# Kernel optimization log

Measured on AMD Instinct MI355X. Metric: run time of the kernel, lower is better.

Reference implementation:

```python
import jax, jax.numpy as jnp
import numpy as np

HIDDEN = 1024

def setup_inputs() -> dict:
    key = jax.random.key(0)
    k1, k2, k3 = jax.random.split(key, 3)
    X = jax.random.normal(k1, (4, 2048, HIDDEN), dtype=jnp.float32)
    W = jax.random.normal(k2, (HIDDEN, 3 * HIDDEN), dtype=jnp.float32) * (1.0 / np.sqrt(HIDDEN))
    b = jax.random.normal(k3, (3 * HIDDEN,), dtype=jnp.float32) * 0.02
    return {"X": X, "W": W, "b": b}

def reference(X, W, b):
    D = X.shape[-1]
    # fused QKV projection: [B,S,3D]
    QKV = jnp.einsum('bsd,de->bse', X, W) + b
    Q, K, V = jnp.split(QKV, 3, axis=-1)
    # full attention scores [B,S,S]
    scores = jnp.einsum('bqd,bkd->bqk', Q, K) / jnp.sqrt(jnp.float32(D))
    attn = jax.nn.softmax(scores, axis=-1)
    out = jnp.einsum('bqk,bkd->bqd', attn, V)
    return out
```

## Files before the change

kernel.cpp:

```cpp
#include <hip/hip_runtime.h>

typedef unsigned short u16;
typedef unsigned int   u32;
typedef __attribute__((ext_vector_type(8)))  short bf16x8;
typedef __attribute__((ext_vector_type(16))) float f32x16;
typedef __attribute__((ext_vector_type(4)))  unsigned short us4;

__device__ __forceinline__ u16 f2bf(float f) {
    union { float f; u32 u; } v; v.f = f;
    u32 u = v.u;
    return (u16)((u + 0x7fffu + ((u >> 16) & 1u)) >> 16);
}
__device__ __forceinline__ float bf2f_lo(u32 p) {
    union { u32 u; float f; } t; t.u = p << 16; return t.f;
}
__device__ __forceinline__ float bf2f_hi(u32 p) {
    union { u32 u; float f; } t; t.u = p & 0xffff0000u; return t.f;
}

__device__ __forceinline__ void gload_lds16(const void* g, void* l) {
    __builtin_amdgcn_global_load_lds((const __attribute__((address_space(1))) u32*)g,
                                     (__attribute__((address_space(3))) u32*)l,
                                     16, 0, 0);
}


template<bool OUT_BF16, bool ADD_BIAS, bool VT_OUT, int MODE>
__global__ __launch_bounds__(256, 2)
void gemm256(const u16* __restrict__ A, int lda, size_t strA,
             const u16* __restrict__ B, int ldb, size_t strB,
             void* __restrict__ Cv, int ldc, size_t strC,
             const float* __restrict__ bias, int K, float alpha)
{
    __shared__ __align__(16) u16 As[256 * 32];
    __shared__ __align__(16) u16 Bs[128 * 32];

    const int tid  = threadIdx.x;
    const int w    = tid >> 6;
    const int lane = tid & 63;
    const int wm   = w >> 1, wn = w & 1;
    const int l31  = lane & 31, lh = lane >> 5;

    const u32 id = blockIdx.x;
    const u32 x  = id & 7, j = id >> 3;
    int mb, nb, bb;
    if (MODE == 0) { bb = 0;      mb = 8 * (j & 3) + x;       nb = j >> 2; }
    else           { bb = x >> 1; mb = 2 * (j & 3) + (x & 1); nb = j >> 2; }
    const int m0 = mb * 256, n0 = nb * 128;

    A += (size_t)bb * strA;
    B += (size_t)bb * strB;

    size_t goffA[4], goffB[2];
#pragma unroll
    for (int h = 0; h < 4; ++h) {
        const int c = h * 256 + w * 64 + lane;
        const int r = c >> 2;
        const int q = ((c & 3) - (r >> 1)) & 3;
        goffA[h] = (size_t)(m0 + r) * lda + q * 8;
    }
#pragma unroll
    for (int h = 0; h < 2; ++h) {
        const int c = h * 256 + w * 64 + lane;
        const int r = c >> 2;
        const int q = ((c & 3) - (r >> 1)) & 3;
        goffB[h] = (size_t)(n0 + r) * ldb + q * 8;
    }

    int offA[4][2], offB[2][2];
#pragma unroll
    for (int i = 0; i < 4; ++i) {
        const int ra = wm * 128 + i * 32 + l31;
#pragma unroll
        for (int ks = 0; ks < 2; ++ks)
            offA[i][ks] = (ra * 4 + ((ks * 2 + lh + (ra >> 1)) & 3)) * 16;
    }
#pragma unroll
    for (int jj = 0; jj < 2; ++jj) {
        const int rb = wn * 64 + jj * 32 + l31;
#pragma unroll
        for (int ks = 0; ks < 2; ++ks)
            offB[jj][ks] = (rb * 4 + ((ks * 2 + lh + (rb >> 1)) & 3)) * 16;
    }

    f32x16 acc[4][2] = {};

    for (int k0 = 0; k0 < K; k0 += 32) {
#pragma unroll
        for (int h = 0; h < 4; ++h)
            gload_lds16(A + goffA[h] + k0, (char*)As + (h * 256 + w * 64) * 16);
#pragma unroll
        for (int h = 0; h < 2; ++h)
            gload_lds16(B + goffB[h] + k0, (char*)Bs + (h * 256 + w * 64) * 16);
        __syncthreads();

        bf16x8 af[4][2], bfr[2][2];
#pragma unroll
        for (int i = 0; i < 4; ++i)
#pragma unroll
            for (int ks = 0; ks < 2; ++ks)
                af[i][ks] = *(const bf16x8*)((const char*)As + offA[i][ks]);
#pragma unroll
        for (int jj = 0; jj < 2; ++jj)
#pragma unroll
            for (int ks = 0; ks < 2; ++ks)
                bfr[jj][ks] = *(const bf16x8*)((const char*)Bs + offB[jj][ks]);

#pragma unroll
        for (int ks = 0; ks < 2; ++ks)
#pragma unroll
            for (int i = 0; i < 4; ++i)
#pragma unroll
                for (int jj = 0; jj < 2; ++jj)
                    acc[i][jj] = __builtin_amdgcn_mfma_f32_32x32x16_bf16(
                        af[i][ks], bfr[jj][ks], acc[i][jj], 0, 0, 0);
        __syncthreads();
    }

    float bval[2];
    if (ADD_BIAS) {
#pragma unroll
        for (int jj = 0; jj < 2; ++jj) bval[jj] = bias[n0 + wn * 64 + jj * 32 + l31];
    }
#pragma unroll
    for (int i = 0; i < 4; ++i) {
        const int rowb = m0 + wm * 128 + i * 32 + 4 * lh;
#pragma unroll
        for (int jj = 0; jj < 2; ++jj) {
            const int col = n0 + wn * 64 + jj * 32 + l31;
            if (VT_OUT) {
                const int b = rowb >> 11;
                u16* dst = (u16*)Cv + ((size_t)(b * 1024) + col) * 2048 + (rowb & 2047);
#pragma unroll
                for (int g = 0; g < 4; ++g) {
                    us4 o = { f2bf(acc[i][jj][4 * g + 0] + bval[jj]),
                              f2bf(acc[i][jj][4 * g + 1] + bval[jj]),
                              f2bf(acc[i][jj][4 * g + 2] + bval[jj]),
                              f2bf(acc[i][jj][4 * g + 3] + bval[jj]) };
                    *(us4*)(dst + 8 * g) = o;
                }
            } else {
#pragma unroll
                for (int r = 0; r < 16; ++r) {
                    const int row = rowb + (r & 3) + 8 * (r >> 2);
                    float v = acc[i][jj][r] * alpha;
                    if (ADD_BIAS) v += bval[jj];
                    if (OUT_BF16)
                        ((u16*)Cv)[(size_t)bb * strC + (size_t)row * ldc + col] = f2bf(v);
                    else
                        ((float*)Cv)[(size_t)bb * strC + (size_t)row * ldc + col] = v;
                }
            }
        }
    }
}

template<bool OUT_BF16>
__global__ __launch_bounds__(256)
void gemm128(const u16* __restrict__ A, int lda, size_t strA,
             const u16* __restrict__ B, int ldb, size_t strB,
             void* __restrict__ Cv, int ldc, size_t strC,
             int K, float alpha)
{
    __shared__ __align__(16) u16 As[128 * 32];
    __shared__ __align__(16) u16 Bs[128 * 32];

    const int tid  = threadIdx.x;
    const int w    = tid >> 6;
    const int lane = tid & 63;
    const int wm   = w >> 1, wn = w & 1;
    const int l31  = lane & 31, lh = lane >> 5;

    const u32 id = blockIdx.x;
    const u32 x  = id & 7, j = id >> 3;
    const int bb = x >> 1;
    const int mb = 2 * (int)(j & 7) + (int)(x & 1);
    const int nb = j >> 3;
    const int m0 = mb * 128, n0 = nb * 128;

    A += (size_t)bb * strA;
    B += (size_t)bb * strB;

    size_t goffA[2], goffB[2];
#pragma unroll
    for (int h = 0; h < 2; ++h) {
        const int c = h * 256 + w * 64 + lane;
        const int r = c >> 2;
        const int q = ((c & 3) - (r >> 1)) & 3;
        goffA[h] = (size_t)(m0 + r) * lda + q * 8;
        goffB[h] = (size_t)(n0 + r) * ldb + q * 8;
    }

    int offA[2][2], offB[2][2];
#pragma unroll
    for (int i = 0; i < 2; ++i) {
        const int ra = wm * 64 + i * 32 + l31;
        const int rb = wn * 64 + i * 32 + l31;
#pragma unroll
        for (int ks = 0; ks < 2; ++ks) {
            const int qq = ks * 2 + lh;
            offA[i][ks] = (ra * 4 + ((qq + (ra >> 1)) & 3)) * 16;
            offB[i][ks] = (rb * 4 + ((qq + (rb >> 1)) & 3)) * 16;
        }
    }

    f32x16 acc[2][2] = {};

    for (int k0 = 0; k0 < K; k0 += 32) {
        gload_lds16(A + goffA[0] + k0, (char*)As + (w * 64) * 16);
        gload_lds16(A + goffA[1] + k0, (char*)As + (256 + w * 64) * 16);
        gload_lds16(B + goffB[0] + k0, (char*)Bs + (w * 64) * 16);
        gload_lds16(B + goffB[1] + k0, (char*)Bs + (256 + w * 64) * 16);
        __syncthreads();

        bf16x8 af[2][2], bfr[2][2];
#pragma unroll
        for (int i = 0; i < 2; ++i)
#pragma unroll
            for (int ks = 0; ks < 2; ++ks) {
                af[i][ks]  = *(const bf16x8*)((const char*)As + offA[i][ks]);
                bfr[i][ks] = *(const bf16x8*)((const char*)Bs + offB[i][ks]);
            }
#pragma unroll
        for (int ks = 0; ks < 2; ++ks)
#pragma unroll
            for (int i = 0; i < 2; ++i)
#pragma unroll
                for (int jj = 0; jj < 2; ++jj)
                    acc[i][jj] = __builtin_amdgcn_mfma_f32_32x32x16_bf16(
                        af[i][ks], bfr[jj][ks], acc[i][jj], 0, 0, 0);
        __syncthreads();
    }

#pragma unroll
    for (int i = 0; i < 2; ++i) {
        const int rowb = m0 + wm * 64 + i * 32 + 4 * lh;
#pragma unroll
        for (int jj = 0; jj < 2; ++jj) {
            const int col = n0 + wn * 64 + jj * 32 + l31;
#pragma unroll
            for (int r = 0; r < 16; ++r) {
                const int row = rowb + (r & 3) + 8 * (r >> 2);
                float v = acc[i][jj][r] * alpha;
                if (OUT_BF16)
                    ((u16*)Cv)[(size_t)bb * strC + (size_t)row * ldc + col] = f2bf(v);
                else
                    ((float*)Cv)[(size_t)bb * strC + (size_t)row * ldc + col] = v;
            }
        }
    }
}

__global__ __launch_bounds__(256)
void convert_x(const float* __restrict__ X, u16* __restrict__ Xb, int n4)
{
    int i = blockIdx.x * blockDim.x + threadIdx.x;
    if (i < n4) {
        float4 v = ((const float4*)X)[i];
        us4 o = { f2bf(v.x), f2bf(v.y), f2bf(v.z), f2bf(v.w) };
        ((us4*)Xb)[i] = o;
    }
}

__global__ __launch_bounds__(256)
void transpose_w(const float* __restrict__ W, u16* __restrict__ Wt)
{
    __shared__ u16 t[64][65];
    const int k0 = blockIdx.x * 64, n0 = blockIdx.y * 64;
    const int tx = threadIdx.x, ty = threadIdx.y;
#pragma unroll
    for (int i = 0; i < 64; i += 4)
        t[ty + i][tx] = f2bf(W[(size_t)(k0 + ty + i) * 3072 + n0 + tx]);
    __syncthreads();
#pragma unroll
    for (int i = 0; i < 64; i += 4)
        Wt[(size_t)(n0 + ty + i) * 1024 + k0 + tx] = t[tx][ty + i];
}

__global__ __launch_bounds__(256)
void softmax_rows(u16* __restrict__ S)
{
    __shared__ float redm[4], reds[4];
    u16* sr = S + (size_t)blockIdx.x * 2048;
    const int t = threadIdx.x;

    uint4 raw = ((const uint4*)sr)[t];
    float xx[8];
    xx[0] = bf2f_lo(raw.x); xx[1] = bf2f_hi(raw.x);
    xx[2] = bf2f_lo(raw.y); xx[3] = bf2f_hi(raw.y);
    xx[4] = bf2f_lo(raw.z); xx[5] = bf2f_hi(raw.z);
    xx[6] = bf2f_lo(raw.w); xx[7] = bf2f_hi(raw.w);

    float mx = fmaxf(fmaxf(fmaxf(xx[0], xx[1]), fmaxf(xx[2], xx[3])),
                     fmaxf(fmaxf(xx[4], xx[5]), fmaxf(xx[6], xx[7])));
#pragma unroll
    for (int o = 32; o; o >>= 1) mx = fmaxf(mx, __shfl_xor(mx, o));
    if ((t & 63) == 0) redm[t >> 6] = mx;
    __syncthreads();
    mx = fmaxf(fmaxf(redm[0], redm[1]), fmaxf(redm[2], redm[3]));

    float e[8], s = 0.f;
#pragma unroll
    for (int k = 0; k < 8; ++k) { e[k] = __expf(xx[k] - mx); s += e[k]; }
#pragma unroll
    for (int o = 32; o; o >>= 1) s += __shfl_xor(s, o);
    if ((t & 63) == 0) reds[t >> 6] = s;
    __syncthreads();
    s = reds[0] + reds[1] + reds[2] + reds[3];
    const float inv = 1.0f / s;

    uint4 o4;
    o4.x = (u32)f2bf(e[0] * inv) | ((u32)f2bf(e[1] * inv) << 16);
    o4.y = (u32)f2bf(e[2] * inv) | ((u32)f2bf(e[3] * inv) << 16);
    o4.z = (u32)f2bf(e[4] * inv) | ((u32)f2bf(e[5] * inv) << 16);
    o4.w = (u32)f2bf(e[6] * inv) | ((u32)f2bf(e[7] * inv) << 16);
    ((uint4*)sr)[t] = o4;
}

extern "C" void kernel_launch(void* const* d_in, const int* in_sizes, int n_in,
                              void* d_out, int out_size, void* d_ws, size_t ws_size,
                              hipStream_t stream)
{
    const float* X    = (const float*)d_in[0];
    const float* W    = (const float*)d_in[1];
    const float* bias = (const float*)d_in[2];
    float* out = (float*)d_out;
    char* ws = (char*)d_ws;

    u16* QK = (u16*)ws;
    u16* Vt = (u16*)(ws + 33554432);
    u16* S  = (u16*)(ws + 50331648);
    u16* Xb = (u16*)(ws + 50331648);
    u16* Wt = (u16*)(ws + 67108864);

    convert_x<<<8192, 256, 0, stream>>>(X, Xb, 8192 * 1024 / 4);
    transpose_w<<<dim3(16, 48), dim3(64, 4), 0, stream>>>(W, Wt);

    gemm256<true, true, false, 0><<<512, 256, 0, stream>>>(
        Xb, 1024, 0, Wt, 1024, 0, QK, 2048, 0, bias, 1024, 1.0f);

    gemm256<true, true, true, 0><<<256, 256, 0, stream>>>(
        Xb, 1024, 0, Wt + (size_t)2048 * 1024, 1024, 0, Vt, 2048, 0,
        bias + 2048, 1024, 1.0f);

    gemm256<true, false, false, 2><<<512, 256, 0, stream>>>(
        QK,        2048, (size_t)2048 * 2048,
        QK + 1024, 2048, (size_t)2048 * 2048,
        S,         2048, (size_t)2048 * 2048,
        nullptr, 1024, 0.03125f);

    softmax_rows<<<8192, 256, 0, stream>>>(S);

    gemm128<false><<<512, 256, 0, stream>>>(
        S,  2048, (size_t)2048 * 2048,
        Vt, 2048, (size_t)1024 * 2048,
        out, 1024, (size_t)2048 * 1024,
        2048, 1.0f);
}
```

Before: 273.7 us.

## Double-buffer GEMM LDS tiles via registers and fuse X fp32-to-bf16 conversion

Replaces the direct global-to-LDS loads in both GEMM kernels with a register-staged, double-buffered pipeline. The next K-tile is fetched into registers while MFMAs run on the current LDS buffer, which removes one barrier per iteration. The QKV projection GEMMs now read fp32 X directly and convert to bf16 in registers, so the separate convert_x kernel and its workspace round trip are gone. The cost is doubled LDS use and higher register pressure, plus re-reading and re-converting fp32 X (twice the bytes) in every tile that loads it.

Result: slower. 424.4 us (+55.0%).

```diff
diff --git a/kernel.cpp b/kernel.cpp
--- a/kernel.cpp
+++ b/kernel.cpp
@@ -11,6 +11,9 @@
     u32 u = v.u;
     return (u16)((u + 0x7fffu + ((u >> 16) & 1u)) >> 16);
 }
+__device__ __forceinline__ u32 pk2bf(float a, float b) {
+    return (u32)f2bf(a) | ((u32)f2bf(b) << 16);
+}
 __device__ __forceinline__ float bf2f_lo(u32 p) {
     union { u32 u; float f; } t; t.u = p << 16; return t.f;
 }
@@ -18,53 +21,42 @@
     union { u32 u; float f; } t; t.u = p & 0xffff0000u; return t.f;
 }
 
-__device__ __forceinline__ void gload_lds16(const void* g, void* l) {
-    __builtin_amdgcn_global_load_lds((const __attribute__((address_space(1))) u32*)g,
-                                     (__attribute__((address_space(3))) u32*)l,
-                                     16, 0, 0);
-}
-
-
-template<bool OUT_BF16, bool ADD_BIAS, bool VT_OUT, int MODE>
+template<bool A_FP32, bool OUT_BF16, bool ADD_BIAS, bool VT_OUT, int MODE>
 __global__ __launch_bounds__(256, 2)
-void gemm256(const u16* __restrict__ A, int lda, size_t strA,
-             const u16* __restrict__ B, int ldb, size_t strB,
-             void* __restrict__ Cv, int ldc, size_t strC,
-             const float* __restrict__ bias, int K, float alpha)
-{
-    __shared__ __align__(16) u16 As[256 * 32];
-    __shared__ __align__(16) u16 Bs[128 * 32];
-
-    const int tid  = threadIdx.x;
-    const int w    = tid >> 6;
-    const int lane = tid & 63;
-    const int wm   = w >> 1, wn = w & 1;
-    const int l31  = lane & 31, lh = lane >> 5;
-
-    const u32 id = blockIdx.x;
-    const u32 x  = id & 7, j = id >> 3;
+void gemm256p(const void* __restrict__ Av, int lda, size_t strA,
+              const u16* __restrict__ Bp, int ldb, size_t strB,
+              void* __restrict__ Cv, int ldc, size_t strC,
+              const float* __restrict__ bias, int K, float alpha)
+{
+    __shared__ __align__(16) u16 As[2][256 * 32];
+    __shared__ __align__(16) u16 Bs[2][128 * 32];
+
+    const int tid = threadIdx.x, w = tid >> 6, lane = tid & 63;
+    const int wm = w >> 1, wn = w & 1, l31 = lane & 31, lh = lane >> 5;
+
+    const u32 id = blockIdx.x, x = id & 7, j = id >> 3;
     int mb, nb, bb;
-    if (MODE == 0) { bb = 0;      mb = 8 * (j & 3) + x;       nb = j >> 2; }
-    else           { bb = x >> 1; mb = 2 * (j & 3) + (x & 1); nb = j >> 2; }
+    if (MODE == 0) { bb = 0;           mb = 8 * (int)(j & 3) + (int)x;       nb = (int)(j >> 2); }
+    else           { bb = (int)(x >> 1); mb = 2 * (int)(j & 3) + (int)(x & 1); nb = (int)(j >> 2); }
     const int m0 = mb * 256, n0 = nb * 128;
 
-    A += (size_t)bb * strA;
-    B += (size_t)bb * strB;
-
-    size_t goffA[4], goffB[2];
-#pragma unroll
-    for (int h = 0; h < 4; ++h) {
-        const int c = h * 256 + w * 64 + lane;
-        const int r = c >> 2;
-        const int q = ((c & 3) - (r >> 1)) & 3;
-        goffA[h] = (size_t)(m0 + r) * lda + q * 8;
-    }
-#pragma unroll
-    for (int h = 0; h < 2; ++h) {
-        const int c = h * 256 + w * 64 + lane;
-        const int r = c >> 2;
-        const int q = ((c & 3) - (r >> 1)) & 3;
-        goffB[h] = (size_t)(n0 + r) * ldb + q * 8;
+    const int esz = A_FP32 ? 4 : 2;
+    const char* Ab = (const char*)Av + (size_t)bb * strA * esz;
+    const u16*  Bb = Bp + (size_t)bb * strB;
+
+    size_t gA[4]; int lA[4];
+#pragma unroll
+    for (int i = 0; i < 4; ++i) {
+        const int c = i * 256 + tid, r = c >> 2, q = c & 3;
+        gA[i] = ((size_t)(m0 + r) * lda + q * 8) * esz;
+        lA[i] = (r * 4 + ((q + (r >> 1)) & 3)) * 16;
+    }
+    size_t gB[2]; int lB[2];
+#pragma unroll
+    for (int i = 0; i < 2; ++i) {
+        const int c = i * 256 + tid, r = c >> 2, q = c & 3;
+        gB[i] = ((size_t)(n0 + r) * ldb + q * 8) * 2;
+        lB[i] = (r * 4 + ((q + (r >> 1)) & 3)) * 16;
     }
 
     int offA[4][2], offB[2][2];
@@ -85,36 +77,75 @@
 
     f32x16 acc[4][2] = {};
 
-    for (int k0 = 0; k0 < K; k0 += 32) {
-#pragma unroll
-        for (int h = 0; h < 4; ++h)
-            gload_lds16(A + goffA[h] + k0, (char*)As + (h * 256 + w * 64) * 16);
-#pragma unroll
-        for (int h = 0; h < 2; ++h)
-            gload_lds16(B + goffB[h] + k0, (char*)Bs + (h * 256 + w * 64) * 16);
+    float4 pa0[4], pa1[4]; uint4 pah[4]; uint4 pbh[2];
+
+#pragma unroll
+    for (int i = 0; i < 4; ++i) {
+        if (A_FP32) { pa0[i] = *(const float4*)(Ab + gA[i]);
+                      pa1[i] = *(const float4*)(Ab + gA[i] + 16); }
+        else          pah[i] = *(const uint4*)(Ab + gA[i]);
+    }
+#pragma unroll
+    for (int i = 0; i < 2; ++i) pbh[i] = *(const uint4*)((const char*)Bb + gB[i]);
+#pragma unroll
+    for (int i = 0; i < 4; ++i) {
+        uint4 v;
+        if (A_FP32) { v.x = pk2bf(pa0[i].x, pa0[i].y); v.y = pk2bf(pa0[i].z, pa0[i].w);
+                      v.z = pk2bf(pa1[i].x, pa1[i].y); v.w = pk2bf(pa1[i].z, pa1[i].w); }
+        else v = pah[i];
+        *(uint4*)((char*)As[0] + lA[i]) = v;
+    }
+#pragma unroll
+    for (int i = 0; i < 2; ++i) *(uint4*)((char*)Bs[0] + lB[i]) = pbh[i];
+
+    int cur = 0;
+    for (int k0 = 32; k0 <= K; k0 += 32) {
+        const bool more = k0 < K;
+        if (more) {
+            const size_t ka = (size_t)k0 * esz, kb = (size_t)k0 * 2;
+#pragma unroll
+            for (int i = 0; i < 4; ++i) {
+                if (A_FP32) { pa0[i] = *(const float4*)(Ab + gA[i] + ka);
+                              pa1[i] = *(const float4*)(Ab + gA[i] + ka + 16); }
+                else          pah[i] = *(const uint4*)(Ab + gA[i] + ka);
+            }
+#pragma unroll
+            for (int i = 0; i < 2; ++i) pbh[i] = *(const uint4*)((const char*)Bb + gB[i] + kb);
+        }
         __syncthreads();
 
-        bf16x8 af[4][2], bfr[2][2];
-#pragma unroll
-        for (int i = 0; i < 4; ++i)
-#pragma unroll
-            for (int ks = 0; ks < 2; ++ks)
-                af[i][ks] = *(const bf16x8*)((const char*)As + offA[i][ks]);
-#pragma unroll
-        for (int jj = 0; jj < 2; ++jj)
-#pragma unroll
-            for (int ks = 0; ks < 2; ++ks)
-                bfr[jj][ks] = *(const bf16x8*)((const char*)Bs + offB[jj][ks]);
-
-#pragma unroll
-        for (int ks = 0; ks < 2; ++ks)
+        const u16* Ac = As[cur]; const u16* Bc = Bs[cur];
+#pragma unroll
+        for (int ks = 0; ks < 2; ++ks) {
+            bf16x8 af[4], bfr[2];
+#pragma unroll
+            for (int i = 0; i < 4; ++i)
+                af[i] = *(const bf16x8*)((const char*)Ac + offA[i][ks]);
+#pragma unroll
+            for (int jj = 0; jj < 2; ++jj)
+                bfr[jj] = *(const bf16x8*)((const char*)Bc + offB[jj][ks]);
 #pragma unroll
             for (int i = 0; i < 4; ++i)
 #pragma unroll
                 for (int jj = 0; jj < 2; ++jj)
                     acc[i][jj] = __builtin_amdgcn_mfma_f32_32x32x16_bf16(
-                        af[i][ks], bfr[jj][ks], acc[i][jj], 0, 0, 0);
-        __syncthreads();
+                        af[i], bfr[jj], acc[i][jj], 0, 0, 0);
+        }
+
+        if (more) {
+            const int nxt = cur ^ 1;
+#pragma unroll
+            for (int i = 0; i < 4; ++i) {
+                uint4 v;
+                if (A_FP32) { v.x = pk2bf(pa0[i].x, pa0[i].y); v.y = pk2bf(pa0[i].z, pa0[i].w);
+                              v.z = pk2bf(pa1[i].x, pa1[i].y); v.w = pk2bf(pa1[i].z, pa1[i].w); }
+                else v = pah[i];
+                *(uint4*)((char*)As[nxt] + lA[i]) = v;
+            }
+#pragma unroll
+            for (int i = 0; i < 2; ++i) *(uint4*)((char*)Bs[nxt] + lB[i]) = pbh[i];
+        }
+        cur ^= 1;
     }
 
     float bval[2];
@@ -157,38 +188,33 @@
 
 template<bool OUT_BF16>
 __global__ __launch_bounds__(256)
-void gemm128(const u16* __restrict__ A, int lda, size_t strA,
-             const u16* __restrict__ B, int ldb, size_t strB,
-             void* __restrict__ Cv, int ldc, size_t strC,
-             int K, float alpha)
-{
-    __shared__ __align__(16) u16 As[128 * 32];
-    __shared__ __align__(16) u16 Bs[128 * 32];
-
-    const int tid  = threadIdx.x;
-    const int w    = tid >> 6;
-    const int lane = tid & 63;
-    const int wm   = w >> 1, wn = w & 1;
-    const int l31  = lane & 31, lh = lane >> 5;
-
-    const u32 id = blockIdx.x;
-    const u32 x  = id & 7, j = id >> 3;
-    const int bb = x >> 1;
+void gemm128p(const u16* __restrict__ Ap, int lda, size_t strA,
+              const u16* __restrict__ Bp, int ldb, size_t strB,
+              void* __restrict__ Cv, int ldc, size_t strC,
+              int K, float alpha)
+{
+    __shared__ __align__(16) u16 As[2][128 * 32];
+    __shared__ __align__(16) u16 Bs[2][128 * 32];
+
+    const int tid = threadIdx.x, w = tid >> 6, lane = tid & 63;
+    const int wm = w >> 1, wn = w & 1, l31 = lane & 31, lh = lane >> 5;
+
+    const u32 id = blockIdx.x, x = id & 7, j = id >> 3;
+    const int bb = (int)(x >> 1);
     const int mb = 2 * (int)(j & 7) + (int)(x & 1);
-    const int nb = j >> 3;
+    const int nb = (int)(j >> 3);
     const int m0 = mb * 128, n0 = nb * 128;
 
-    A += (size_t)bb * strA;
-    B += (size_t)bb * strB;
-
-    size_t goffA[2], goffB[2];
-#pragma unroll
-    for (int h = 0; h < 2; ++h) {
-        const int c = h * 256 + w * 64 + lane;
-        const int r = c >> 2;
-        const int q = ((c & 3) - (r >> 1)) & 3;
-        goffA[h] = (size_t)(m0 + r) * lda + q * 8;
-        goffB[h] = (size_t)(n0 + r) * ldb + q * 8;
+    const u16* Ab = Ap + (size_t)bb * strA;
+    const u16* Bb = Bp + (size_t)bb * strB;
+
+    size_t gA[2], gB[2]; int lA[2], lB[2];
+#pragma unroll
+    for (int i = 0; i < 2; ++i) {
+        const int c = i * 256 + tid, r = c >> 2, q = c & 3;
+        gA[i] = ((size_t)(m0 + r) * lda + q * 8) * 2;
+        gB[i] = ((size_t)(n0 + r) * ldb + q * 8) * 2;
+        lA[i] = lB[i] = (r * 4 + ((q + (r >> 1)) & 3)) * 16;
     }
 
     int offA[2][2], offB[2][2];
@@ -198,38 +224,64 @@
         const int rb = wn * 64 + i * 32 + l31;
 #pragma unroll
         for (int ks = 0; ks < 2; ++ks) {
-            const int qq = ks * 2 + lh;
-            offA[i][ks] = (ra * 4 + ((qq + (ra >> 1)) & 3)) * 16;
-            offB[i][ks] = (rb * 4 + ((qq + (rb >> 1)) & 3)) * 16;
+            offA[i][ks] = (ra * 4 + ((ks * 2 + lh + (ra >> 1)) & 3)) * 16;
+            offB[i][ks] = (rb * 4 + ((ks * 2 + lh + (rb >> 1)) & 3)) * 16;
         }
     }
 
     f32x16 acc[2][2] = {};
-
-    for (int k0 = 0; k0 < K; k0 += 32) {
-        gload_lds16(A + goffA[0] + k0, (char*)As + (w * 64) * 16);
-        gload_lds16(A + goffA[1] + k0, (char*)As + (256 + w * 64) * 16);
-        gload_lds16(B + goffB[0] + k0, (char*)Bs + (w * 64) * 16);
-        gload_lds16(B + goffB[1] + k0, (char*)Bs + (256 + w * 64) * 16);
+    uint4 pah[2], pbh[2];
+
+#pragma unroll
+    for (int i = 0; i < 2; ++i) {
+        pah[i] = *(const uint4*)((const char*)Ab + gA[i]);
+        pbh[i] = *(const uint4*)((const char*)Bb + gB[i]);
+    }
+#pragma unroll
+    for (int i = 0; i < 2; ++i) {
+        *(uint4*)((char*)As[0] + lA[i]) = pah[i];
+        *(uint4*)((char*)Bs[0] + lB[i]) = pbh[i];
+    }
+
+    int cur = 0;
+    for (int k0 = 32; k0 <= K; k0 += 32) {
+        const bool more = k0 < K;
+        if (more) {
+            const size_t kb = (size_t)k0 * 2;
+#pragma unroll
+            for (int i = 0; i < 2; ++i) {
+                pah[i] = *(const uint4*)((const char*)Ab + gA[i] + kb);
+                pbh[i] = *(const uint4*)((const char*)Bb + gB[i] + kb);
+            }
+        }
         __syncthreads();
 
-        bf16x8 af[2][2], bfr[2][2];
-#pragma unroll
-        for (int i = 0; i < 2; ++i)
-#pragma unroll
-            for (int ks = 0; ks < 2; ++ks) {
-                af[i][ks]  = *(const bf16x8*)((const char*)As + offA[i][ks]);
-                bfr[i][ks] = *(const bf16x8*)((const char*)Bs + offB[i][ks]);
-            }
-#pragma unroll
-        for (int ks = 0; ks < 2; ++ks)
+        const u16* Ac = As[cur]; const u16* Bc = Bs[cur];
+#pragma unroll
+        for (int ks = 0; ks < 2; ++ks) {
+            bf16x8 af[2], bfr[2];
+#pragma unroll
+            for (int i = 0; i < 2; ++i) {
+                af[i]  = *(const bf16x8*)((const char*)Ac + offA[i][ks]);
+                bfr[i] = *(const bf16x8*)((const char*)Bc + offB[i][ks]);
+            }
 #pragma unroll
             for (int i = 0; i < 2; ++i)
 #pragma unroll
                 for (int jj = 0; jj < 2; ++jj)
                     acc[i][jj] = __builtin_amdgcn_mfma_f32_32x32x16_bf16(
-                        af[i][ks], bfr[jj][ks], acc[i][jj], 0, 0, 0);
-        __syncthreads();
+                        af[i], bfr[jj], acc[i][jj], 0, 0, 0);
+        }
+
+        if (more) {
+            const int nxt = cur ^ 1;
+#pragma unroll
+            for (int i = 0; i < 2; ++i) {
+                *(uint4*)((char*)As[nxt] + lA[i]) = pah[i];
+                *(uint4*)((char*)Bs[nxt] + lB[i]) = pbh[i];
+            }
+        }
+        cur ^= 1;
     }
 
 #pragma unroll
@@ -252,17 +304,6 @@
 }
 
 __global__ __launch_bounds__(256)
-void convert_x(const float* __restrict__ X, u16* __restrict__ Xb, int n4)
-{
-    int i = blockIdx.x * blockDim.x + threadIdx.x;
-    if (i < n4) {
-        float4 v = ((const float4*)X)[i];
-        us4 o = { f2bf(v.x), f2bf(v.y), f2bf(v.z), f2bf(v.w) };
-        ((us4*)Xb)[i] = o;
-    }
-}
-
-__global__ __launch_bounds__(256)
 void transpose_w(const float* __restrict__ W, u16* __restrict__ Wt)
 {
     __shared__ u16 t[64][65];
@@ -330,20 +371,18 @@
     u16* QK = (u16*)ws;
     u16* Vt = (u16*)(ws + 33554432);
     u16* S  = (u16*)(ws + 50331648);
-    u16* Xb = (u16*)(ws + 50331648);
-    u16* Wt = (u16*)(ws + 67108864);
-
-    convert_x<<<8192, 256, 0, stream>>>(X, Xb, 8192 * 1024 / 4);
+    u16* Wt = (u16*)(ws + 50331648);
+
     transpose_w<<<dim3(16, 48), dim3(64, 4), 0, stream>>>(W, Wt);
 
-    gemm256<true, true, false, 0><<<512, 256, 0, stream>>>(
-        Xb, 1024, 0, Wt, 1024, 0, QK, 2048, 0, bias, 1024, 1.0f);
-
-    gemm256<true, true, true, 0><<<256, 256, 0, stream>>>(
-        Xb, 1024, 0, Wt + (size_t)2048 * 1024, 1024, 0, Vt, 2048, 0,
+    gemm256p<true, true, true, false, 0><<<512, 256, 0, stream>>>(
+        X, 1024, 0, Wt, 1024, 0, QK, 2048, 0, bias, 1024, 1.0f);
+
+    gemm256p<true, true, true, true, 0><<<256, 256, 0, stream>>>(
+        X, 1024, 0, Wt + (size_t)2048 * 1024, 1024, 0, Vt, 2048, 0,
         bias + 2048, 1024, 1.0f);
 
-    gemm256<true, false, false, 2><<<512, 256, 0, stream>>>(
+    gemm256p<false, true, false, false, 2><<<512, 256, 0, stream>>>(
         QK,        2048, (size_t)2048 * 2048,
         QK + 1024, 2048, (size_t)2048 * 2048,
         S,         2048, (size_t)2048 * 2048,
@@ -351,7 +390,7 @@
 
     softmax_rows<<<8192, 256, 0, stream>>>(S);
 
-    gemm128<false><<<512, 256, 0, stream>>>(
+    gemm128p<false><<<512, 256, 0, stream>>>(
         S,  2048, (size_t)2048 * 2048,
         Vt, 2048, (size_t)1024 * 2048,
         out, 1024, (size_t)2048 * 1024,
```

## Double-buffer LDS tiles in GEMM kernels to overlap loads with MFMA

Applied to the files above, without the earlier changes.

Both GEMM kernels now keep two LDS buffers per operand. The first k-tile is prefetched before the loop, and each iteration issues the next tile's direct-to-LDS global loads before running MFMAs on the current buffer. One barrier per iteration replaces the previous two, so global memory latency is meant to hide behind matrix math. The cost is doubled shared memory per block, which could limit occupancy, and correctness depends on the barrier waiting for the async LDS loads to finish.

After: 279.7 us. 2.2% more time.

```diff
diff --git a/kernel.cpp b/kernel.cpp
--- a/kernel.cpp
+++ b/kernel.cpp
@@ -23,7 +23,6 @@
                                      (__attribute__((address_space(3))) u32*)l,
                                      16, 0, 0);
 }
-
 
 template<bool OUT_BF16, bool ADD_BIAS, bool VT_OUT, int MODE>
 __global__ __launch_bounds__(256, 2)
@@ -32,8 +31,8 @@
              void* __restrict__ Cv, int ldc, size_t strC,
              const float* __restrict__ bias, int K, float alpha)
 {
-    __shared__ __align__(16) u16 As[256 * 32];
-    __shared__ __align__(16) u16 Bs[128 * 32];
+    __shared__ __align__(16) u16 As[2][256 * 32];
+    __shared__ __align__(16) u16 Bs[2][128 * 32];
 
     const int tid  = threadIdx.x;
     const int w    = tid >> 6;
@@ -41,11 +40,10 @@
     const int wm   = w >> 1, wn = w & 1;
     const int l31  = lane & 31, lh = lane >> 5;
 
-    const u32 id = blockIdx.x;
-    const u32 x  = id & 7, j = id >> 3;
+    const u32 id = blockIdx.x, x = id & 7, j = id >> 3;
     int mb, nb, bb;
-    if (MODE == 0) { bb = 0;      mb = 8 * (j & 3) + x;       nb = j >> 2; }
-    else           { bb = x >> 1; mb = 2 * (j & 3) + (x & 1); nb = j >> 2; }
+    if (MODE == 0) { bb = 0;             mb = 8 * (int)(j & 3) + (int)x;        nb = (int)(j >> 2); }
+    else           { bb = (int)(x >> 1); mb = 2 * (int)(j & 3) + (int)(x & 1);  nb = (int)(j >> 2); }
     const int m0 = mb * 256, n0 = nb * 128;
 
     A += (size_t)bb * strA;
@@ -85,36 +83,45 @@
 
     f32x16 acc[4][2] = {};
 
+#pragma unroll
+    for (int h = 0; h < 4; ++h)
+        gload_lds16(A + goffA[h], (char*)As[0] + (h * 256 + w * 64) * 16);
+#pragma unroll
+    for (int h = 0; h < 2; ++h)
+        gload_lds16(B + goffB[h], (char*)Bs[0] + (h * 256 + w * 64) * 16);
+
+    int cur = 0;
     for (int k0 = 0; k0 < K; k0 += 32) {
-#pragma unroll
-        for (int h = 0; h < 4; ++h)
-            gload_lds16(A + goffA[h] + k0, (char*)As + (h * 256 + w * 64) * 16);
-#pragma unroll
-        for (int h = 0; h < 2; ++h)
-            gload_lds16(B + goffB[h] + k0, (char*)Bs + (h * 256 + w * 64) * 16);
         __syncthreads();
 
-        bf16x8 af[4][2], bfr[2][2];
-#pragma unroll
-        for (int i = 0; i < 4; ++i)
-#pragma unroll
-            for (int ks = 0; ks < 2; ++ks)
-                af[i][ks] = *(const bf16x8*)((const char*)As + offA[i][ks]);
-#pragma unroll
-        for (int jj = 0; jj < 2; ++jj)
-#pragma unroll
-            for (int ks = 0; ks < 2; ++ks)
-                bfr[jj][ks] = *(const bf16x8*)((const char*)Bs + offB[jj][ks]);
-
-#pragma unroll
-        for (int ks = 0; ks < 2; ++ks)
+        const int nk = k0 + 32;
+        if (nk < K) {
+#pragma unroll
+            for (int h = 0; h < 4; ++h)
+                gload_lds16(A + goffA[h] + nk, (char*)As[cur ^ 1] + (h * 256 + w * 64) * 16);
+#pragma unroll
+            for (int h = 0; h < 2; ++h)
+                gload_lds16(B + goffB[h] + nk, (char*)Bs[cur ^ 1] + (h * 256 + w * 64) * 16);
+        }
+
+        const u16* Ac = As[cur]; const u16* Bc = Bs[cur];
+#pragma unroll
+        for (int ks = 0; ks < 2; ++ks) {
+            bf16x8 af[4], bfr[2];
+#pragma unroll
+            for (int i = 0; i < 4; ++i)
+                af[i] = *(const bf16x8*)((const char*)Ac + offA[i][ks]);
+#pragma unroll
+            for (int jj = 0; jj < 2; ++jj)
+                bfr[jj] = *(const bf16x8*)((const char*)Bc + offB[jj][ks]);
 #pragma unroll
             for (int i = 0; i < 4; ++i)
 #pragma unroll
                 for (int jj = 0; jj < 2; ++jj)
                     acc[i][jj] = __builtin_amdgcn_mfma_f32_32x32x16_bf16(
-                        af[i][ks], bfr[jj][ks], acc[i][jj], 0, 0, 0);
-        __syncthreads();
+                        af[i], bfr[jj], acc[i][jj], 0, 0, 0);
+        }
+        cur ^= 1;
     }
 
     float bval[2];
@@ -162,8 +169,8 @@
              void* __restrict__ Cv, int ldc, size_t strC,
              int K, float alpha)
 {
-    __shared__ __align__(16) u16 As[128 * 32];
-    __shared__ __align__(16) u16 Bs[128 * 32];
+    __shared__ __align__(16) u16 As[2][128 * 32];
+    __shared__ __align__(16) u16 Bs[2][128 * 32];
 
     const int tid  = threadIdx.x;
     const int w    = tid >> 6;
@@ -171,11 +178,10 @@
     const int wm   = w >> 1, wn = w & 1;
     const int l31  = lane & 31, lh = lane >> 5;
 
-    const u32 id = blockIdx.x;
-    const u32 x  = id & 7, j = id >> 3;
-    const int bb = x >> 1;
+    const u32 id = blockIdx.x, x = id & 7, j = id >> 3;
+    const int bb = (int)(x >> 1);
     const int mb = 2 * (int)(j & 7) + (int)(x & 1);
-    const int nb = j >> 3;
+    const int nb = (int)(j >> 3);
     const int m0 = mb * 128, n0 = nb * 128;
 
     A += (size_t)bb * strA;
@@ -206,30 +212,42 @@
 
     f32x16 acc[2][2] = {};
 
+#pragma unroll
+    for (int h = 0; h < 2; ++h) {
+        gload_lds16(A + goffA[h], (char*)As[0] + (h * 256 + w * 64) * 16);
+        gload_lds16(B + goffB[h], (char*)Bs[0] + (h * 256 + w * 64) * 16);
+    }
+
+    int cur = 0;
     for (int k0 = 0; k0 < K; k0 += 32) {
-        gload_lds16(A + goffA[0] + k0, (char*)As + (w * 64) * 16);
-        gload_lds16(A + goffA[1] + k0, (char*)As + (256 + w * 64) * 16);
-        gload_lds16(B + goffB[0] + k0, (char*)Bs + (w * 64) * 16);
-        gload_lds16(B + goffB[1] + k0, (char*)Bs + (256 + w * 64) * 16);
         __syncthreads();
 
-        bf16x8 af[2][2], bfr[2][2];
-#pragma unroll
-        for (int i = 0; i < 2; ++i)
-#pragma unroll
-            for (int ks = 0; ks < 2; ++ks) {
-                af[i][ks]  = *(const bf16x8*)((const char*)As + offA[i][ks]);
-                bfr[i][ks] = *(const bf16x8*)((const char*)Bs + offB[i][ks]);
+        const int nk = k0 + 32;
+        if (nk < K) {
+#pragma unroll
+            for (int h = 0; h < 2; ++h) {
+                gload_lds16(A + goffA[h] + nk, (char*)As[cur ^ 1] + (h * 256 + w * 64) * 16);
+                gload_lds16(B + goffB[h] + nk, (char*)Bs[cur ^ 1] + (h * 256 + w * 64) * 16);
             }
-#pragma unroll
-        for (int ks = 0; ks < 2; ++ks)
+        }
+
+        const u16* Ac = As[cur]; const u16* Bc = Bs[cur];
+#pragma unroll
+        for (int ks = 0; ks < 2; ++ks) {
+            bf16x8 af[2], bfr[2];
+#pragma unroll
+            for (int i = 0; i < 2; ++i) {
+                af[i]  = *(const bf16x8*)((const char*)Ac + offA[i][ks]);
+                bfr[i] = *(const bf16x8*)((const char*)Bc + offB[i][ks]);
+            }
 #pragma unroll
             for (int i = 0; i < 2; ++i)
 #pragma unroll
                 for (int jj = 0; jj < 2; ++jj)
                     acc[i][jj] = __builtin_amdgcn_mfma_f32_32x32x16_bf16(
-                        af[i][ks], bfr[jj][ks], acc[i][jj], 0, 0, 0);
-        __syncthreads();
+                        af[i], bfr[jj], acc[i][jj], 0, 0, 0);
+        }
+        cur ^= 1;
     }
 
 #pragma unroll
```
